# Performance work log

Hardware: AMD Instinct MI355X
Metric: run time of the kernel (lower is better)

The kernel has to match this reference:

```python
import jax, jax.numpy as jnp
import numpy as np

N = 100000   # nodes
F_IN = 128   # node features
H = 32       # hidden size (hard-coded in module)


def setup_inputs() -> dict:
    key = jax.random.key(0)
    ks = jax.random.split(key, 20)
    inp = {
        'x': jax.random.normal(ks[0], (N, F_IN), dtype=jnp.float32),
        'edge_index': jax.random.randint(ks[1], (2, 3200000), 0, N, dtype=jnp.int64),
        'edge_weight': jax.random.uniform(ks[2], (3200000,), dtype=jnp.float32),
        'prev_hidden_state': jax.random.normal(ks[3], (N, H), dtype=jnp.float32),
    }
    s = 1.0 / np.sqrt(F_IN)
    s2 = 1.0 / np.sqrt(2 * H)
    sh = 1.0 / np.sqrt(H)
    # GCNConv weights (in->H) + bias, for gates z, r, h
    for i, g in enumerate(['z', 'r', 'h']):
        inp[f'Wc_{g}'] = jax.random.uniform(ks[4 + i], (F_IN, H), minval=-s, maxval=s, dtype=jnp.float32)
        inp[f'bc_{g}'] = jnp.zeros((H,), dtype=jnp.float32)
        # torch Linear(2H -> H): weight [H, 2H], bias [H]
        inp[f'Wl_{g}'] = jax.random.uniform(ks[8 + i], (H, 2 * H), minval=-s2, maxval=s2, dtype=jnp.float32)
        inp[f'bl_{g}'] = jax.random.uniform(ks[12 + i], (H,), minval=-s2, maxval=s2, dtype=jnp.float32)
    inp['W_head'] = jax.random.uniform(ks[16], (1, H), minval=-sh, maxval=sh, dtype=jnp.float32)
    inp['b_head'] = jax.random.uniform(ks[17], (1,), minval=-sh, maxval=sh, dtype=jnp.float32)
    return inp


def _gcn_norm(edge_index, edge_weight):
    # add self-loops with weight 1, symmetric GCN normalization
    loop = jnp.arange(N, dtype=edge_index.dtype)
    row = jnp.concatenate([edge_index[0], loop])
    col = jnp.concatenate([edge_index[1], loop])
    w = jnp.concatenate([edge_weight, jnp.ones((N,), dtype=edge_weight.dtype)])
    deg = jax.ops.segment_sum(w, col, num_segments=N)
    dinv = jnp.where(deg > 0, jax.lax.rsqrt(jnp.where(deg > 0, deg, 1.0)), 0.0)
    norm = dinv[row] * w * dinv[col]
    return row, col, norm


def _gcn_conv(x, W, b, row, col, norm):
    xw = x @ W                                   # [N, H]
    agg = jax.ops.segment_sum(norm[:, None] * xw[row], col, num_segments=N)
    return agg + b


def reference(x, edge_index, edge_weight, prev_hidden_state,
              Wc_z, bc_z, Wl_z, bl_z,
              Wc_r, bc_r, Wl_r, bl_r,
              Wc_h, bc_h, Wl_h, bl_h,
              W_head, b_head):
    row, col, norm = _gcn_norm(edge_index, edge_weight)
    Hprev = prev_hidden_state

    cz = _gcn_conv(x, Wc_z, bc_z, row, col, norm)
    Z = jax.nn.sigmoid(jnp.concatenate([cz, Hprev], axis=1) @ Wl_z.T + bl_z)

    cr = _gcn_conv(x, Wc_r, bc_r, row, col, norm)
    R = jax.nn.sigmoid(jnp.concatenate([cr, Hprev], axis=1) @ Wl_r.T + bl_r)

    ch = _gcn_conv(x, Wc_h, bc_h, row, col, norm)
    Ht = jnp.tanh(jnp.concatenate([ch, Hprev * R], axis=1) @ Wl_h.T + bl_h)

    Hnew = Z * Hprev + (1.0 - Z) * Ht
    y = jax.nn.relu(Hnew) @ W_head.T + b_head    # [N, 1]
    return (y, Hnew)
```

## Files before the change

### kernel.cpp

```cpp
#include <hip/hip_runtime.h>

#define NN 100000
#define FIN 128
#define HD 32
#define EE 3200000
#define NBUK 391
#define EPB 16384
#define NBLK ((EE + EPB - 1) / EPB)

typedef unsigned int uint;
typedef unsigned short ushort;

__device__ __forceinline__ ushort f2bf(float f) {
    uint b = __float_as_uint(f);
    return (ushort)((b + 0x7FFFu + ((b >> 16) & 1u)) >> 16);
}
__device__ __forceinline__ float bf2f(ushort u) {
    return __uint_as_float(((uint)u) << 16);
}

__global__ void detect_kernel(const uint* __restrict__ ei32, int* __restrict__ flag) {
    int t = threadIdx.x;
    uint v = 0;
#pragma unroll
    for (int r = 0; r < 4; r++) v |= ei32[2 * (t + 64 * r) + 1];
    unsigned long long nz = __ballot(v != 0u);
    if (t == 0) *flag = (nz == 0ULL) ? 1 : 0;
}

__device__ __forceinline__ int load_idx32(const int* __restrict__ ei, long long pos, int is64) {
    return is64 ? ei[pos * 2] : ei[pos];
}

__global__ __launch_bounds__(256) void passA_hist(const int* __restrict__ ei,
                                                  int* __restrict__ blockhist,
                                                  const int* __restrict__ flag) {
    __shared__ int hist[NBUK];
    int tid = threadIdx.x, blk = blockIdx.x;
    for (int b = tid; b < NBUK; b += 256) hist[b] = 0;
    __syncthreads();
    int is64 = *flag;
    int e0 = blk * EPB, e1 = e0 + EPB; if (e1 > EE) e1 = EE;
    for (int e = e0 + tid; e < e1; e += 256) {
        int col = load_idx32(ei, (long long)EE + e, is64);
        atomicAdd(&hist[col >> 8], 1);
    }
    __syncthreads();
    for (int b = tid; b < NBUK; b += 256) blockhist[blk * NBUK + b] = hist[b];
}

__global__ void scan_bucket(const int* __restrict__ blockhist, int* __restrict__ off_local,
                            int* __restrict__ total) {
    int b = blockIdx.x;
    int l = threadIdx.x;
    int run = 0;
    for (int c = 0; c < NBLK; c += 64) {
        int blk = c + l;
        int v = (blk < NBLK) ? blockhist[blk * NBUK + b] : 0;
        int incl = v;
#pragma unroll
        for (int d = 1; d < 64; d <<= 1) {
            int t = __shfl_up(incl, d, 64);
            if (l >= d) incl += t;
        }
        if (blk < NBLK) off_local[blk * NBUK + b] = run + (incl - v);
        run += __shfl(incl, 63, 64);
    }
    if (l == 0) total[b] = run;
}

__global__ void scan_total(const int* __restrict__ total, int* __restrict__ bstart) {
    __shared__ int sd[512];
    int t = threadIdx.x;
    int v = (t < NBUK) ? total[t] : 0;
    sd[t] = v;
    __syncthreads();
    for (int off = 1; off < 512; off <<= 1) {
        int x = (t >= off) ? sd[t - off] : 0;
        __syncthreads();
        sd[t] += x;
        __syncthreads();
    }
    if (t < NBUK) bstart[t] = sd[t] - v;
    if (t == NBUK - 1) bstart[NBUK] = sd[t];
}

__global__ __launch_bounds__(256) void passC_scatter(const int* __restrict__ ei,
                                                     const float* __restrict__ wt,
                                                     const int* __restrict__ bstart,
                                                     const int* __restrict__ off_local,
                                                     uint2* __restrict__ erec2,
                                                     const int* __restrict__ flag) {
    __shared__ int cur[NBUK];
    int tid = threadIdx.x, blk = blockIdx.x;
    for (int b = tid; b < NBUK; b += 256) cur[b] = bstart[b] + off_local[blk * NBUK + b];
    __syncthreads();
    int is64 = *flag;
    int e0 = blk * EPB, e1 = e0 + EPB; if (e1 > EE) e1 = EE;
    for (int e = e0 + tid; e < e1; e += 256) {
        int row = load_idx32(ei, e, is64);
        int col = load_idx32(ei, (long long)EE + e, is64);
        uint nb = __float_as_uint(wt[e]);
        uint enc = ((nb + 0x8000u) >> 16) & 0x7FFFu;
        int pos = atomicAdd(&cur[col >> 8], 1);
        uint2 r; r.x = (uint)row | (enc << 17); r.y = (uint)(col & 255);
        erec2[pos] = r;
    }
}

__global__ __launch_bounds__(256) void passB_fine(const uint2* __restrict__ erec2,
                                                  const int* __restrict__ bstart,
                                                  uint* __restrict__ erecF,
                                                  int* __restrict__ estart, int* __restrict__ cnt,
                                                  float* __restrict__ dinv) {
    __shared__ int hist[256];
    __shared__ float wsum[256];
    __shared__ int off[256];
    __shared__ int cur[256];
    __shared__ int sd[256];
    int t = threadIdx.x, b = blockIdx.x;
    hist[t] = 0; wsum[t] = 0.f;
    __syncthreads();
    int e0 = bstart[b], e1 = bstart[b + 1];
    for (int e = e0 + t; e < e1; e += 256) {
        uint2 r = erec2[e];
        int cl = (int)r.y;
        atomicAdd(&hist[cl], 1);
        atomicAdd(&wsum[cl], __uint_as_float((r.x >> 17) << 16));
    }
    __syncthreads();
    int v = hist[t];
    sd[t] = v;
    __syncthreads();
    for (int o = 1; o < 256; o <<= 1) {
        int x = (t >= o) ? sd[t - o] : 0;
        __syncthreads();
        sd[t] += x;
        __syncthreads();
    }
    off[t] = sd[t] - v;
    cur[t] = 0;
    int node = b * 256 + t;
    if (node < NN) {
        estart[node] = e0 + off[t];
        cnt[node] = v;
        dinv[node] = rsqrtf(1.0f + wsum[t]);
    }
    __syncthreads();
    for (int e = e0 + t; e < e1; e += 256) {
        uint2 r = erec2[e];
        int cl = (int)r.y;
        int p = atomicAdd(&cur[cl], 1);
        erecF[e0 + off[cl] + p] = r.x;
    }
}

__global__ __launch_bounds__(256) void gemm_xw_kernel(
        const float* __restrict__ x,
        const float* __restrict__ Wz, const float* __restrict__ Wr, const float* __restrict__ Wh,
        ushort* __restrict__ xw16) {
    __shared__ float Bs[128 * 96];
    __shared__ float AsT[8 * 128];
    int tid = threadIdx.x;
    int tx = tid & 31, ty = tid >> 5;
    int rowBase = blockIdx.x * 128;

    for (int e = tid; e < 4096; e += 256) { int k = e >> 5, c = e & 31; Bs[k * 96 + c]      = Wz[e]; }
    for (int e = tid; e < 4096; e += 256) { int k = e >> 5, c = e & 31; Bs[k * 96 + 32 + c] = Wr[e]; }
    for (int e = tid; e < 4096; e += 256) { int k = e >> 5, c = e & 31; Bs[k * 96 + 64 + c] = Wh[e]; }

    float acc0[16], acc1[16], acc2[16];
#pragma unroll
    for (int r = 0; r < 16; r++) { acc0[r] = 0.f; acc1[r] = 0.f; acc2[r] = 0.f; }

    int lr = tid >> 1;
    int lc = (tid & 1) * 4;
    for (int k0 = 0; k0 < 128; k0 += 8) {
        __syncthreads();
        int gr = rowBase + lr;
        float4 a4 = make_float4(0.f, 0.f, 0.f, 0.f);
        if (gr < NN) a4 = *(const float4*)(x + (long long)gr * FIN + k0 + lc);
        AsT[(lc + 0) * 128 + lr] = a4.x;
        AsT[(lc + 1) * 128 + lr] = a4.y;
        AsT[(lc + 2) * 128 + lr] = a4.z;
        AsT[(lc + 3) * 128 + lr] = a4.w;
        __syncthreads();
#pragma unroll
        for (int kk = 0; kk < 8; kk++) {
            float b0 = Bs[(k0 + kk) * 96 + tx];
            float b1 = Bs[(k0 + kk) * 96 + 32 + tx];
            float b2 = Bs[(k0 + kk) * 96 + 64 + tx];
            const float4* ap = (const float4*)(AsT + kk * 128 + ty * 16);
            float4 a0 = ap[0], a1 = ap[1], a2 = ap[2], a3 = ap[3];
            float av[16] = {a0.x,a0.y,a0.z,a0.w, a1.x,a1.y,a1.z,a1.w,
                            a2.x,a2.y,a2.z,a2.w, a3.x,a3.y,a3.z,a3.w};
#pragma unroll
            for (int r = 0; r < 16; r++) {
                acc0[r] = fmaf(av[r], b0, acc0[r]);
                acc1[r] = fmaf(av[r], b1, acc1[r]);
                acc2[r] = fmaf(av[r], b2, acc2[r]);
            }
        }
    }
#pragma unroll
    for (int r = 0; r < 16; r++) {
        int gr = rowBase + ty * 16 + r;
        if (gr < NN) {
            ushort* o = xw16 + (long long)gr * 96;
            uint zr = (uint)f2bf(acc0[r]) | ((uint)f2bf(acc1[r]) << 16);
            *(uint*)(o + 2 * tx) = zr;
            o[64 + tx] = f2bf(acc2[r]);
        }
    }
}

__global__ __launch_bounds__(512) void agg_gate_kernel(
        const uint* __restrict__ erecF, const int* __restrict__ estart, const int* __restrict__ cnt,
        const ushort* __restrict__ xw16, const float* __restrict__ dinv,
        const float* __restrict__ hprev,
        const float* __restrict__ bcz, const float* __restrict__ bcr, const float* __restrict__ bch,
        const float* __restrict__ Wlz, const float* __restrict__ blz,
        const float* __restrict__ Wlr, const float* __restrict__ blr,
        const float* __restrict__ Wlh, const float* __restrict__ blh,
        const float* __restrict__ Whead, const float* __restrict__ bhead,
        float* __restrict__ y, float* __restrict__ hnew) {
    __shared__ float WzT[64 * 32], WrT[64 * 32], WhT[64 * 32];
    __shared__ float czs[16][32], crs[16][32], chs[16][32], hps[16][32], rhs[16][32];
    __shared__ uint2 rw[16][32];
    int tid = threadIdx.x;
    for (int e2 = tid; e2 < 2048; e2 += 512) {
        int jj = e2 >> 6, k = e2 & 63;
        WzT[k * 32 + jj] = Wlz[e2];
        WrT[k * 32 + jj] = Wlr[e2];
        WhT[k * 32 + jj] = Wlh[e2];
    }
    int s = tid >> 5, j = tid & 31;
    int i = blockIdx.x * 16 + s;
    int beg = estart[i], c = cnt[i], end = beg + c;

    float cz = 0.f, cr = 0.f, ch = 0.f;
    for (int base = beg; base < end; base += 32) {
        int e = base + j;
        if (e < end) {
            uint v = erecF[e];
            int row = (int)(v & 0x1FFFFu);
            float w = __uint_as_float((v >> 17) << 16);
            uint2 q; q.x = (uint)row; q.y = __float_as_uint(w * dinv[row]);
            rw[s][j] = q;
        }
        int mm = end - base; if (mm > 32) mm = 32;
        int t = 0;
        for (; t + 4 <= mm; t += 4) {
            uint2 q0 = rw[s][t], q1 = rw[s][t + 1], q2 = rw[s][t + 2], q3 = rw[s][t + 3];
            const ushort* p0 = xw16 + (long long)q0.x * 96;
            const ushort* p1 = xw16 + (long long)q1.x * 96;
            const ushort* p2 = xw16 + (long long)q2.x * 96;
            const ushort* p3 = xw16 + (long long)q3.x * 96;
            uint a0 = *(const uint*)(p0 + 2 * j);
            uint a1 = *(const uint*)(p1 + 2 * j);
            uint a2 = *(const uint*)(p2 + 2 * j);
            uint a3 = *(const uint*)(p3 + 2 * j);
            ushort h0 = p0[64 + j], h1 = p1[64 + j], h2 = p2[64 + j], h3 = p3[64 + j];
            float w0 = __uint_as_float(q0.y), w1 = __uint_as_float(q1.y);
            float w2 = __uint_as_float(q2.y), w3 = __uint_as_float(q3.y);
            cz = fmaf(w0, __uint_as_float(a0 << 16), cz);
            cr = fmaf(w0, __uint_as_float(a0 & 0xFFFF0000u), cr);
            ch = fmaf(w0, bf2f(h0), ch);
            cz = fmaf(w1, __uint_as_float(a1 << 16), cz);
            cr = fmaf(w1, __uint_as_float(a1 & 0xFFFF0000u), cr);
            ch = fmaf(w1, bf2f(h1), ch);
            cz = fmaf(w2, __uint_as_float(a2 << 16), cz);
            cr = fmaf(w2, __uint_as_float(a2 & 0xFFFF0000u), cr);
            ch = fmaf(w2, bf2f(h2), ch);
            cz = fmaf(w3, __uint_as_float(a3 << 16), cz);
            cr = fmaf(w3, __uint_as_float(a3 & 0xFFFF0000u), cr);
            ch = fmaf(w3, bf2f(h3), ch);
        }
        for (; t < mm; t++) {
            uint2 q = rw[s][t];
            const ushort* xr = xw16 + (long long)q.x * 96;
            uint zr = *(const uint*)(xr + 2 * j);
            float fh = bf2f(xr[64 + j]);
            float w = __uint_as_float(q.y);
            cz = fmaf(w, __uint_as_float(zr << 16), cz);
            cr = fmaf(w, __uint_as_float(zr & 0xFFFF0000u), cr);
            ch = fmaf(w, fh, ch);
        }
    }
    float di = dinv[i], sl = di * di;
    const ushort* xi = xw16 + (long long)i * 96;
    uint zri = *(const uint*)(xi + 2 * j);
    czs[s][j] = fmaf(sl, __uint_as_float(zri << 16),         di * cz) + bcz[j];
    crs[s][j] = fmaf(sl, __uint_as_float(zri & 0xFFFF0000u), di * cr) + bcr[j];
    chs[s][j] = fmaf(sl, bf2f(xi[64 + j]),                   di * ch) + bch[j];
    float hp = hprev[(long long)i * HD + j];
    hps[s][j] = hp;
    __syncthreads();

    float az = blz[j], arv = blr[j];
#pragma unroll
    for (int k = 0; k < 32; k++) {
        az  = fmaf(WzT[k * 32 + j], czs[s][k], az);
        arv = fmaf(WrT[k * 32 + j], crs[s][k], arv);
    }
#pragma unroll
    for (int k = 0; k < 32; k++) {
        float v = hps[s][k];
        az  = fmaf(WzT[(k + 32) * 32 + j], v, az);
        arv = fmaf(WrT[(k + 32) * 32 + j], v, arv);
    }
    float Z = 1.f / (1.f + __expf(-az));
    float R = 1.f / (1.f + __expf(-arv));
    rhs[s][j] = hp * R;
    __syncthreads();

    float ah = blh[j];
#pragma unroll
    for (int k = 0; k < 32; k++) ah = fmaf(WhT[k * 32 + j], chs[s][k], ah);
#pragma unroll
    for (int k = 0; k < 32; k++) ah = fmaf(WhT[(k + 32) * 32 + j], rhs[s][k], ah);
    float Ht = tanhf(ah);
    float hn = Z * hp + (1.f - Z) * Ht;
    float yv = fmaxf(hn, 0.f) * Whead[j];
#pragma unroll
    for (int m = 16; m; m >>= 1) yv += __shfl_xor(yv, m, 32);
    hnew[(long long)i * HD + j] = hn;
    if (j == 0) y[i] = yv + bhead[0];
}

extern "C" void kernel_launch(void* const* d_in, const int* in_sizes, int n_in,
                              void* d_out, int out_size, void* d_ws, size_t ws_size,
                              hipStream_t stream) {
    const float* x     = (const float*)d_in[0];
    const int*   ei    = (const int*)d_in[1];
    const float* wt    = (const float*)d_in[2];
    const float* hprev = (const float*)d_in[3];
    const float* Wcz = (const float*)d_in[4],  *bcz = (const float*)d_in[5];
    const float* Wlz = (const float*)d_in[6],  *blz = (const float*)d_in[7];
    const float* Wcr = (const float*)d_in[8],  *bcr = (const float*)d_in[9];
    const float* Wlr = (const float*)d_in[10], *blr = (const float*)d_in[11];
    const float* Wch = (const float*)d_in[12], *bch = (const float*)d_in[13];
    const float* Wlh = (const float*)d_in[14], *blh = (const float*)d_in[15];
    const float* Whead = (const float*)d_in[16], *bhead = (const float*)d_in[17];

    float* out_y = (float*)d_out;
    float* out_h = (float*)d_out + NN;

    float* ws = (float*)d_ws;
    float* dinv      = ws;
    int*   estart    = (int*)(ws + NN);
    int*   cnt       = (int*)(ws + 2LL * NN);
    int*   bstart    = (int*)(ws + 3LL * NN);
    int*   total     = (int*)(ws + 3LL * NN + 512);
    int*   blockhist = (int*)(ws + 3LL * NN + 1024);
    int*   off_local = (int*)(ws + 3LL * NN + 81024);
    int*   flag      = (int*)(ws + 3LL * NN + 161024);
    ushort* xw16     = (ushort*)(ws + 3LL * NN + 161056);
    uint2*  erec2    = (uint2*)(ws + 51LL * NN + 161056);
    uint*   erecF    = (uint*)(ws + 51LL * NN + 161056 + 2LL * EE);

    detect_kernel<<<1, 64, 0, stream>>>((const uint*)ei, flag);
    passA_hist<<<NBLK, 256, 0, stream>>>(ei, blockhist, flag);
    scan_bucket<<<NBUK, 64, 0, stream>>>(blockhist, off_local, total);
    scan_total<<<1, 512, 0, stream>>>(total, bstart);
    passC_scatter<<<NBLK, 256, 0, stream>>>(ei, wt, bstart, off_local, erec2, flag);
    passB_fine<<<NBUK, 256, 0, stream>>>(erec2, bstart, erecF, estart, cnt, dinv);
    gemm_xw_kernel<<<(NN + 127) / 128, 256, 0, stream>>>(x, Wcz, Wcr, Wch, xw16);
    agg_gate_kernel<<<NN / 16, 512, 0, stream>>>(
        erecF, estart, cnt, xw16, dinv, hprev, bcz, bcr, bch,
        Wlz, blz, Wlr, blr, Wlh, blh, Whead, bhead, out_y, out_h);
}
```

Before: 480.2 us.

## Sort edge records locally in LDS before scatter and prefold dinv into weights

Result: faster. 456.4 us (-5.0%).

```diff
diff --git a/kernel.cpp b/kernel.cpp
--- a/kernel.cpp
+++ b/kernel.cpp
@@ -5,7 +5,7 @@
 #define HD 32
 #define EE 3200000
 #define NBUK 391
-#define EPB 16384
+#define EPB 6144
 #define NBLK ((EE + EPB - 1) / EPB)
 
 typedef unsigned int uint;
@@ -85,15 +85,32 @@
     if (t == NBUK - 1) bstart[NBUK] = sd[t];
 }
 
-__global__ __launch_bounds__(256) void passC_scatter(const int* __restrict__ ei,
-                                                     const float* __restrict__ wt,
-                                                     const int* __restrict__ bstart,
-                                                     const int* __restrict__ off_local,
-                                                     uint2* __restrict__ erec2,
-                                                     const int* __restrict__ flag) {
-    __shared__ int cur[NBUK];
+__global__ __launch_bounds__(256) void sortC_kernel(const int* __restrict__ ei,
+                                                    const float* __restrict__ wt,
+                                                    const int* __restrict__ bstart,
+                                                    const int* __restrict__ off_local,
+                                                    const int* __restrict__ blockhist,
+                                                    uint2* __restrict__ erec2,
+                                                    const int* __restrict__ flag) {
+    __shared__ uint2 lrec[EPB];
+    __shared__ int lstart[NBUK];
+    __shared__ int lcur[NBUK];
     int tid = threadIdx.x, blk = blockIdx.x;
-    for (int b = tid; b < NBUK; b += 256) cur[b] = bstart[b] + off_local[blk * NBUK + b];
+    if (tid < 64) {
+        int run = 0;
+        for (int c = 0; c < NBUK; c += 64) {
+            int b = c + tid;
+            int v = (b < NBUK) ? blockhist[blk * NBUK + b] : 0;
+            int incl = v;
+#pragma unroll
+            for (int d = 1; d < 64; d <<= 1) {
+                int t2 = __shfl_up(incl, d, 64);
+                if (tid >= d) incl += t2;
+            }
+            if (b < NBUK) { lstart[b] = run + incl - v; lcur[b] = run + incl - v; }
+            run += __shfl(incl, 63, 64);
+        }
+    }
     __syncthreads();
     int is64 = *flag;
     int e0 = blk * EPB, e1 = e0 + EPB; if (e1 > EE) e1 = EE;
@@ -102,9 +119,17 @@
         int col = load_idx32(ei, (long long)EE + e, is64);
         uint nb = __float_as_uint(wt[e]);
         uint enc = ((nb + 0x8000u) >> 16) & 0x7FFFu;
-        int pos = atomicAdd(&cur[col >> 8], 1);
-        uint2 r; r.x = (uint)row | (enc << 17); r.y = (uint)(col & 255);
-        erec2[pos] = r;
+        int pos = atomicAdd(&lcur[col >> 8], 1);
+        uint2 r; r.x = (uint)row | (enc << 17); r.y = (uint)col;
+        lrec[pos] = r;
+    }
+    __syncthreads();
+    int m = e1 - e0;
+    for (int slot = tid; slot < m; slot += 256) {
+        uint2 r = lrec[slot];
+        int b = (int)(r.y >> 8);
+        int gpos = bstart[b] + off_local[blk * NBUK + b] + (slot - lstart[b]);
+        erec2[gpos] = r;
     }
 }
 
@@ -124,7 +149,7 @@
     int e0 = bstart[b], e1 = bstart[b + 1];
     for (int e = e0 + t; e < e1; e += 256) {
         uint2 r = erec2[e];
-        int cl = (int)r.y;
+        int cl = (int)(r.y & 255u);
         atomicAdd(&hist[cl], 1);
         atomicAdd(&wsum[cl], __uint_as_float((r.x >> 17) << 16));
     }
@@ -149,10 +174,22 @@
     __syncthreads();
     for (int e = e0 + t; e < e1; e += 256) {
         uint2 r = erec2[e];
-        int cl = (int)r.y;
+        int cl = (int)(r.y & 255u);
         int p = atomicAdd(&cur[cl], 1);
         erecF[e0 + off[cl] + p] = r.x;
     }
+}
+
+__global__ void fixup_kernel(uint* __restrict__ erecF, const float* __restrict__ dinv) {
+    int e = blockIdx.x * blockDim.x + threadIdx.x;
+    if (e >= EE) return;
+    uint v = erecF[e];
+    int row = (int)(v & 0x1FFFFu);
+    float w = __uint_as_float((v >> 17) << 16);
+    float wd = w * dinv[row];
+    uint nb = __float_as_uint(wd);
+    uint enc = ((nb + 0x8000u) >> 16) & 0x7FFFu;
+    erecF[e] = (uint)row | (enc << 17);
 }
 
 __global__ __launch_bounds__(256) void gemm_xw_kernel(
@@ -226,7 +263,7 @@
         float* __restrict__ y, float* __restrict__ hnew) {
     __shared__ float WzT[64 * 32], WrT[64 * 32], WhT[64 * 32];
     __shared__ float czs[16][32], crs[16][32], chs[16][32], hps[16][32], rhs[16][32];
-    __shared__ uint2 rw[16][32];
+    __shared__ uint rwsh[16][32];
     int tid = threadIdx.x;
     for (int e2 = tid; e2 < 2048; e2 += 512) {
         int jj = e2 >> 6, k = e2 & 63;
@@ -239,30 +276,29 @@
     int beg = estart[i], c = cnt[i], end = beg + c;
 
     float cz = 0.f, cr = 0.f, ch = 0.f;
+    int e = beg + j;
+    uint vcur = (e < end) ? erecF[e] : 0u;
     for (int base = beg; base < end; base += 32) {
-        int e = base + j;
-        if (e < end) {
-            uint v = erecF[e];
-            int row = (int)(v & 0x1FFFFu);
-            float w = __uint_as_float((v >> 17) << 16);
-            uint2 q; q.x = (uint)row; q.y = __float_as_uint(w * dinv[row]);
-            rw[s][j] = q;
-        }
+        rwsh[s][j] = vcur;
+        int en = base + 32 + j;
+        uint vnext = (en < end) ? erecF[en] : 0u;
         int mm = end - base; if (mm > 32) mm = 32;
         int t = 0;
         for (; t + 4 <= mm; t += 4) {
-            uint2 q0 = rw[s][t], q1 = rw[s][t + 1], q2 = rw[s][t + 2], q3 = rw[s][t + 3];
-            const ushort* p0 = xw16 + (long long)q0.x * 96;
-            const ushort* p1 = xw16 + (long long)q1.x * 96;
-            const ushort* p2 = xw16 + (long long)q2.x * 96;
-            const ushort* p3 = xw16 + (long long)q3.x * 96;
+            uint v0 = rwsh[s][t], v1 = rwsh[s][t + 1], v2 = rwsh[s][t + 2], v3 = rwsh[s][t + 3];
+            const ushort* p0 = xw16 + (long long)(v0 & 0x1FFFFu) * 96;
+            const ushort* p1 = xw16 + (long long)(v1 & 0x1FFFFu) * 96;
+            const ushort* p2 = xw16 + (long long)(v2 & 0x1FFFFu) * 96;
+            const ushort* p3 = xw16 + (long long)(v3 & 0x1FFFFu) * 96;
             uint a0 = *(const uint*)(p0 + 2 * j);
             uint a1 = *(const uint*)(p1 + 2 * j);
             uint a2 = *(const uint*)(p2 + 2 * j);
             uint a3 = *(const uint*)(p3 + 2 * j);
             ushort h0 = p0[64 + j], h1 = p1[64 + j], h2 = p2[64 + j], h3 = p3[64 + j];
-            float w0 = __uint_as_float(q0.y), w1 = __uint_as_float(q1.y);
-            float w2 = __uint_as_float(q2.y), w3 = __uint_as_float(q3.y);
+            float w0 = __uint_as_float((v0 >> 17) << 16);
+            float w1 = __uint_as_float((v1 >> 17) << 16);
+            float w2 = __uint_as_float((v2 >> 17) << 16);
+            float w3 = __uint_as_float((v3 >> 17) << 16);
             cz = fmaf(w0, __uint_as_float(a0 << 16), cz);
             cr = fmaf(w0, __uint_as_float(a0 & 0xFFFF0000u), cr);
             ch = fmaf(w0, bf2f(h0), ch);
@@ -277,15 +313,16 @@
             ch = fmaf(w3, bf2f(h3), ch);
         }
         for (; t < mm; t++) {
-            uint2 q = rw[s][t];
-            const ushort* xr = xw16 + (long long)q.x * 96;
+            uint v = rwsh[s][t];
+            const ushort* xr = xw16 + (long long)(v & 0x1FFFFu) * 96;
             uint zr = *(const uint*)(xr + 2 * j);
             float fh = bf2f(xr[64 + j]);
-            float w = __uint_as_float(q.y);
+            float w = __uint_as_float((v >> 17) << 16);
             cz = fmaf(w, __uint_as_float(zr << 16), cz);
             cr = fmaf(w, __uint_as_float(zr & 0xFFFF0000u), cr);
             ch = fmaf(w, fh, ch);
         }
+        vcur = vnext;
     }
     float di = dinv[i], sl = di * di;
     const ushort* xi = xw16 + (long long)i * 96;
@@ -353,19 +390,20 @@
     int*   bstart    = (int*)(ws + 3LL * NN);
     int*   total     = (int*)(ws + 3LL * NN + 512);
     int*   blockhist = (int*)(ws + 3LL * NN + 1024);
-    int*   off_local = (int*)(ws + 3LL * NN + 81024);
-    int*   flag      = (int*)(ws + 3LL * NN + 161024);
-    ushort* xw16     = (ushort*)(ws + 3LL * NN + 161056);
-    uint2*  erec2    = (uint2*)(ws + 51LL * NN + 161056);
-    uint*   erecF    = (uint*)(ws + 51LL * NN + 161056 + 2LL * EE);
+    int*   off_local = (int*)(ws + 3LL * NN + 205024);
+    int*   flag      = (int*)(ws + 3LL * NN + 409024);
+    ushort* xw16     = (ushort*)(ws + 3LL * NN + 409056);
+    uint2*  erec2    = (uint2*)(ws + 51LL * NN + 409056);
+    uint*   erecF    = (uint*)(ws + 51LL * NN + 409056 + 2LL * EE);
 
     detect_kernel<<<1, 64, 0, stream>>>((const uint*)ei, flag);
     passA_hist<<<NBLK, 256, 0, stream>>>(ei, blockhist, flag);
     scan_bucket<<<NBUK, 64, 0, stream>>>(blockhist, off_local, total);
     scan_total<<<1, 512, 0, stream>>>(total, bstart);
-    passC_scatter<<<NBLK, 256, 0, stream>>>(ei, wt, bstart, off_local, erec2, flag);
+    sortC_kernel<<<NBLK, 256, 0, stream>>>(ei, wt, bstart, off_local, blockhist, erec2, flag);
     passB_fine<<<NBUK, 256, 0, stream>>>(erec2, bstart, erecF, estart, cnt, dinv);
     gemm_xw_kernel<<<(NN + 127) / 128, 256, 0, stream>>>(x, Wcz, Wcr, Wch, xw16);
+    fixup_kernel<<<(EE + 255) / 256, 256, 0, stream>>>(erecF, dinv);
     agg_gate_kernel<<<NN / 16, 512, 0, stream>>>(
         erecF, estart, cnt, xw16, dinv, hprev, bcz, bcr, bch,
         Wlz, blz, Wlr, blr, Wlh, blh, Whead, bhead, out_y, out_h);
```
